# Kernel optimization log

Measured on AMD Instinct MI355X. Metric: run time of the kernel, lower is better.

The kernel has to match this reference:

```python
import jax, jax.numpy as jnp
import numpy as np

# D2Q9 lattice velocities (standard ordering: rest, axis, diagonal)
E = np.array([[0,0],[1,0],[0,1],[-1,0],[0,-1],[1,1],[-1,1],[-1,-1],[1,-1]], dtype=np.int64)

# Gram-Schmidt moment matrix, row order matches the layer's eq stack:
# [rho, jx, jy, e, eps, qx, qy, pxx, pxy]
_M_np = np.array([
    [ 1,  1,  1,  1,  1,  1,  1,  1,  1],  # rho
    [ 0,  1,  0, -1,  0,  1, -1, -1,  1],  # jx
    [ 0,  0,  1,  0, -1,  1,  1, -1, -1],  # jy
    [-4, -1, -1, -1, -1,  2,  2,  2,  2],  # e
    [ 4, -2, -2, -2, -2,  1,  1,  1,  1],  # eps
    [ 0, -2,  0,  2,  0,  1, -1, -1,  1],  # qx
    [ 0,  0, -2,  0,  2,  1,  1, -1, -1],  # qy
    [ 0,  1, -1,  1, -1,  0,  0,  0,  0],  # pxx
    [ 0,  0,  0,  0,  0,  1, -1,  1, -1],  # pxy
], dtype=np.float64)
_Minv_np = np.linalg.inv(_M_np)

TAU = 0.6
GX, GY = 0.0, -1e-4
ITERATIONS = 4
NX, NY = 1024, 1024


def _stream(f):
    # periodic streaming: shift each population along its lattice velocity
    return jnp.stack(
        [jnp.roll(f[..., i], (int(E[i, 0]), int(E[i, 1])), axis=(0, 1)) for i in range(9)],
        axis=-1,
    )


def setup_inputs() -> dict:
    key = jax.random.key(0)
    kf, kw = jax.random.split(key)
    f = jax.random.uniform(kf, (NX, NY, 9), dtype=jnp.float32)
    w = jax.random.normal(kw, (7,), dtype=jnp.float32)
    return {"f": f, "w": w}


def reference(f, w):
    M = jnp.asarray(_M_np, dtype=f.dtype)
    Minv = jnp.asarray(_Minv_np, dtype=f.dtype)
    ex = jnp.asarray(E[:, 0], dtype=f.dtype)
    ey = jnp.asarray(E[:, 1], dtype=f.dtype)
    inv_tau = jnp.asarray(1.0 / TAU, dtype=f.dtype)

    for _ in range(ITERATIONS):
        # handle_boundaries: periodic (no solid nodes) -> no-op
        f = _stream(f)
        # macroscopic fields
        rho = jnp.sum(f, axis=-1)                      # [X,Y]
        vx = jnp.einsum("xyq,q->xy", f, ex) / rho
        vy = jnp.einsum("xyq,q->xy", f, ey) / rho
        # equilibrium moments with learned coefficients (gravity forcing via tau shift)
        ux = vx + TAU * GX * rho
        uy = vy + TAU * GY * rho
        jx = rho * ux
        jy = rho * uy
        j2 = jx * jx + jy * jy
        e_m = w[0] * rho + w[1] * j2
        eps = w[2] * rho - w[3] * j2
        qx = w[4] * jx
        qy = w[4] * jy
        pxx = w[5] * (jx * jx - jy * jy)
        pxy = w[6] * jx * jy
        meq = jnp.stack([rho, jx, jy, e_m, eps, qx, qy, pxx, pxy], axis=2)
        # collision in moment space, single relaxation rate 1/tau
        m = jnp.einsum("xyq,pq->xyp", f, M)
        m = m - inv_tau * (m - meq)
        f = jnp.einsum("xyp,qp->xyq", m, Minv)
    return f
```

## Files before the change

### kernel.cpp

```cpp
#include <hip/hip_runtime.h>


#define NXD 1024
#define NYD 1024
#define NCELL (NXD * NYD)
#define ROWF (NYD * 9)

constexpr float INV_TAU = (float)(1.0 / 0.6);
constexpr float TGY     = (float)(0.6 * -1e-4);

__device__ __forceinline__ void collide1(
    float f0, float f1, float f2, float f3, float f4,
    float f5, float f6, float f7, float f8,
    float w0, float w1, float w2, float w3, float w4, float w5, float w6,
    float& o0, float& o1, float& o2, float& o3, float& o4,
    float& o5, float& o6, float& o7, float& o8)
{
    const float rho = f0 + f1 + f2 + f3 + f4 + f5 + f6 + f7 + f8;
    const float jx0 = f1 - f3 + f5 - f6 - f7 + f8;
    const float jy0 = f2 - f4 + f5 + f6 - f7 - f8;
    const float vx = jx0 / rho;
    const float vy = jy0 / rho;
    const float uy = vy + TGY * rho;
    const float jx = rho * vx;
    const float jy = rho * uy;
    const float j2 = jx * jx + jy * jy;

    const float ax = f1 + f2 + f3 + f4;
    const float dg = f5 + f6 + f7 + f8;
    const float m3 = -4.f * f0 - ax + 2.f * dg;
    const float m4 =  4.f * f0 - 2.f * ax + dg;
    const float m5 = -2.f * f1 + 2.f * f3 + f5 - f6 - f7 + f8;
    const float m6 = -2.f * f2 + 2.f * f4 + f5 + f6 - f7 - f8;
    const float m7 = f1 - f2 + f3 - f4;
    const float m8 = f5 - f6 + f7 - f8;

    const float me3 = w0 * rho + w1 * j2;
    const float me4 = w2 * rho - w3 * j2;
    const float me5 = w4 * jx;
    const float me6 = w4 * jy;
    const float me7 = w5 * (jx * jx - jy * jy);
    const float me8 = w6 * (jx * jy);

    const float mp1 = jx0 - INV_TAU * (jx0 - jx);
    const float mp2 = jy0 - INV_TAU * (jy0 - jy);
    const float mp3 = m3  - INV_TAU * (m3 - me3);
    const float mp4 = m4  - INV_TAU * (m4 - me4);
    const float mp5 = m5  - INV_TAU * (m5 - me5);
    const float mp6 = m6  - INV_TAU * (m6 - me6);
    const float mp7 = m7  - INV_TAU * (m7 - me7);
    const float mp8 = m8  - INV_TAU * (m8 - me8);

    const float s0 = rho * (1.f / 9.f);
    const float s1 = mp1 * (1.f / 6.f);
    const float s2 = mp2 * (1.f / 6.f);
    const float s3 = mp3 * (1.f / 36.f);
    const float s4 = mp4 * (1.f / 36.f);
    const float s5 = mp5 * (1.f / 12.f);
    const float s6 = mp6 * (1.f / 12.f);
    const float s7 = mp7 * 0.25f;
    const float s8 = mp8 * 0.25f;

    const float h0 = s0 - s3 - 2.f * s4;
    const float g0 = s0 + 2.f * s3 + s4;

    o0 = s0 - 4.f * s3 + 4.f * s4;
    o1 = h0 + s1 - 2.f * s5 + s7;
    o2 = h0 + s2 - 2.f * s6 - s7;
    o3 = h0 - s1 + 2.f * s5 + s7;
    o4 = h0 - s2 + 2.f * s6 - s7;
    o5 = g0 + s1 + s2 + s5 + s6 + s8;
    o6 = g0 - s1 + s2 - s5 + s6 - s8;
    o7 = g0 - s1 - s2 - s5 - s6 + s8;
    o8 = g0 + s1 - s2 + s5 - s6 - s8;
}

__device__ __forceinline__ void collide4(const float4 (&F)[9], float4 (&O)[9],
                                         const float (&w)[7]) {
    #pragma unroll
    for (int j = 0; j < 4; ++j) {
        float f[9], o[9];
        #pragma unroll
        for (int q = 0; q < 9; ++q)
            f[q] = ((const float*)&F[q])[j];
        collide1(f[0], f[1], f[2], f[3], f[4], f[5], f[6], f[7], f[8],
                 w[0], w[1], w[2], w[3], w[4], w[5], w[6],
                 o[0], o[1], o[2], o[3], o[4], o[5], o[6], o[7], o[8]);
        #pragma unroll
        for (int q = 0; q < 9; ++q)
            ((float*)&O[q])[j] = o[q];
    }
}

__device__ __forceinline__ float4 ld4s(const float* __restrict__ rowp, int yb) {
    if (yb >= 0 && yb + 3 < NYD) {
        float4 v;
        __builtin_memcpy(&v, rowp + yb, sizeof(float4));
        return v;
    }
    float4 v;
    v.x = rowp[(yb + 0) & (NYD - 1)];
    v.y = rowp[(yb + 1) & (NYD - 1)];
    v.z = rowp[(yb + 2) & (NYD - 1)];
    v.w = rowp[(yb + 3) & (NYD - 1)];
    return v;
}

__device__ __forceinline__ void pull_loads(const float* __restrict__ src,
                                           int x, int y0, float4 (&F)[9]) {
    const int xm = (x - 1) & (NXD - 1), xp = (x + 1) & (NXD - 1);
    const float* p0 = src + 0 * NCELL + x  * NYD;
    const float* p1 = src + 1 * NCELL + xm * NYD;
    const float* p2 = src + 2 * NCELL + x  * NYD;
    const float* p3 = src + 3 * NCELL + xp * NYD;
    const float* p4 = src + 4 * NCELL + x  * NYD;
    const float* p5 = src + 5 * NCELL + xm * NYD;
    const float* p6 = src + 6 * NCELL + xp * NYD;
    const float* p7 = src + 7 * NCELL + xp * NYD;
    const float* p8 = src + 8 * NCELL + xm * NYD;
    __builtin_memcpy(&F[0], p0 + y0, sizeof(float4));
    __builtin_memcpy(&F[1], p1 + y0, sizeof(float4));
    __builtin_memcpy(&F[3], p3 + y0, sizeof(float4));
    F[2] = ld4s(p2, y0 - 1);
    F[5] = ld4s(p5, y0 - 1);
    F[6] = ld4s(p6, y0 - 1);
    F[4] = ld4s(p4, y0 + 1);
    F[7] = ld4s(p7, y0 + 1);
    F[8] = ld4s(p8, y0 + 1);
}

__device__ __forceinline__ void load_w(const float* __restrict__ wp,
                                       float (&w)[7]) {
    #pragma unroll
    for (int i = 0; i < 7; ++i) w[i] = wp[i];
}

__global__ __launch_bounds__(256) void k1_sc(const float* __restrict__ src,
                                             float* __restrict__ dst,
                                             const float* __restrict__ wp) {
    __shared__ float L[3][258 * 9];
    const int b   = blockIdx.x;
    const int x   = b >> 2;
    const int y0  = (b & 3) << 8;
    const int tid = threadIdx.x;

    #pragma unroll
    for (int r = 0; r < 3; ++r) {
        const int srow = (x - 1 + r) & (NXD - 1);
        const float* rb = src + (size_t)srow * ROWF;
        const int base = y0 * 9 - 9;
        for (int p = tid; p < 258 * 9; p += 256) {
            int fr = base + p;
            if (fr < 0) fr += ROWF;
            else if (fr >= ROWF) fr -= ROWF;
            L[r][p] = rb[fr];
        }
    }
    __syncthreads();

    float w[7];
    load_w(wp, w);

    const int ly = tid;
    const int y  = y0 + ly;
    const float f0 = L[1][(ly + 1) * 9 + 0];
    const float f1 = L[0][(ly + 1) * 9 + 1];
    const float f2 = L[1][(ly + 0) * 9 + 2];
    const float f3 = L[2][(ly + 1) * 9 + 3];
    const float f4 = L[1][(ly + 2) * 9 + 4];
    const float f5 = L[0][(ly + 0) * 9 + 5];
    const float f6 = L[2][(ly + 0) * 9 + 6];
    const float f7 = L[2][(ly + 2) * 9 + 7];
    const float f8 = L[0][(ly + 2) * 9 + 8];

    float o0,o1,o2,o3,o4,o5,o6,o7,o8;
    collide1(f0,f1,f2,f3,f4,f5,f6,f7,f8,
             w[0],w[1],w[2],w[3],w[4],w[5],w[6],
             o0,o1,o2,o3,o4,o5,o6,o7,o8);

    const int c = x * NYD + y;
    dst[0 * NCELL + c] = o0;
    dst[1 * NCELL + c] = o1;
    dst[2 * NCELL + c] = o2;
    dst[3 * NCELL + c] = o3;
    dst[4 * NCELL + c] = o4;
    dst[5 * NCELL + c] = o5;
    dst[6 * NCELL + c] = o6;
    dst[7 * NCELL + c] = o7;
    dst[8 * NCELL + c] = o8;
}

__global__ __launch_bounds__(256) void k_sc(const float* __restrict__ src,
                                            float* __restrict__ dst,
                                            const float* __restrict__ wp) {
    const int x  = blockIdx.x;
    const int y0 = threadIdx.x << 2;

    float4 F[9];
    pull_loads(src, x, y0, F);

    float w[7];
    load_w(wp, w);

    float4 O[9];
    collide4(F, O, w);

    const int c = x * NYD + y0;
    #pragma unroll
    for (int q = 0; q < 9; ++q)
        *(float4*)(dst + q * NCELL + c) = O[q];
}

__global__ __launch_bounds__(256) void k_sc_aos(const float* __restrict__ src,
                                                float* __restrict__ dst,
                                                const float* __restrict__ wp) {
    __shared__ float4 T[ROWF / 4];
    const int x   = blockIdx.x;
    const int tid = threadIdx.x;
    const int y0  = tid << 2;

    float4 F[9];
    pull_loads(src, x, y0, F);

    float w[7];
    load_w(wp, w);

    float4 O[9];
    collide4(F, O, w);

    float* t = (float*)(T + tid * 9);
    #pragma unroll
    for (int j = 0; j < 4; ++j) {
        #pragma unroll
        for (int q = 0; q < 9; ++q)
            t[j * 9 + q] = ((const float*)&O[q])[j];
    }
    __syncthreads();

    float4* dv = (float4*)(dst + (size_t)x * ROWF);
    #pragma unroll
    for (int it = 0; it < 9; ++it)
        dv[tid + it * 256] = T[tid + it * 256];
}

__global__ __launch_bounds__(256) void lbm_step_aos(const float* __restrict__ src,
                                                    float* __restrict__ dst,
                                                    const float* __restrict__ wp) {
    const int cell = blockIdx.x * 256 + threadIdx.x;
    const int x = cell >> 10;
    const int y = cell & (NYD - 1);
    const int xm = (x + NXD - 1) & (NXD - 1);
    const int xp = (x + 1) & (NXD - 1);
    const int ym = (y + NYD - 1) & (NYD - 1);
    const int yp = (y + 1) & (NYD - 1);

    const float f0 = src[(x  * NYD + y ) * 9 + 0];
    const float f1 = src[(xm * NYD + y ) * 9 + 1];
    const float f2 = src[(x  * NYD + ym) * 9 + 2];
    const float f3 = src[(xp * NYD + y ) * 9 + 3];
    const float f4 = src[(x  * NYD + yp) * 9 + 4];
    const float f5 = src[(xm * NYD + ym) * 9 + 5];
    const float f6 = src[(xp * NYD + ym) * 9 + 6];
    const float f7 = src[(xp * NYD + yp) * 9 + 7];
    const float f8 = src[(xm * NYD + yp) * 9 + 8];

    float o0,o1,o2,o3,o4,o5,o6,o7,o8;
    collide1(f0,f1,f2,f3,f4,f5,f6,f7,f8,
             wp[0],wp[1],wp[2],wp[3],wp[4],wp[5],wp[6],
             o0,o1,o2,o3,o4,o5,o6,o7,o8);

    float* o = dst + (size_t)(x * NYD + y) * 9;
    o[0]=o0; o[1]=o1; o[2]=o2; o[3]=o3; o[4]=o4; o[5]=o5; o[6]=o6; o[7]=o7; o[8]=o8;
}

extern "C" void kernel_launch(void* const* d_in, const int* in_sizes, int n_in,
                              void* d_out, int out_size, void* d_ws, size_t ws_size,
                              hipStream_t stream) {
    const float* f_in = (const float*)d_in[0];
    const float* w    = (const float*)d_in[1];
    float* out = (float*)d_out;
    float* A   = (float*)d_ws;
    const size_t bufBytes = (size_t)NCELL * 9 * sizeof(float);

    if (ws_size >= 2 * bufBytes) {
        float* B = A + (size_t)NCELL * 9;
        k1_sc   <<<4096, 256, 0, stream>>>(f_in, A, w);
        k_sc    <<<1024, 256, 0, stream>>>(A, B, w);
        k_sc    <<<1024, 256, 0, stream>>>(B, A, w);
        k_sc_aos<<<1024, 256, 0, stream>>>(A, out, w);
    } else {
        float* fin_mut = (float*)d_in[0];
        lbm_step_aos<<<4096, 256, 0, stream>>>(f_in, out, w);
        lbm_step_aos<<<4096, 256, 0, stream>>>(out, fin_mut, w);
        lbm_step_aos<<<4096, 256, 0, stream>>>(fin_mut, out, w);
        lbm_step_aos<<<4096, 256, 0, stream>>>(out, fin_mut, w);
        hipMemcpyAsync(d_out, fin_mut, bufBytes, hipMemcpyDeviceToDevice, stream);
    }
}
```

Baseline: 164.0 us.

## Switch from pull-stream-collide to push collide-stream with separate transpose kernel

Replaces the pull-based stream+collide kernels with a push scheme: the first kernel only transposes AoS input to SoA while streaming, then collide-and-push kernels read aligned float4 rows and write shifted outputs, using shared memory to exchange the y-boundary lanes. Reads become fully aligned and unconditional, removing misaligned and wraparound pull loads. The cost is one extra full-grid launch (5 kernels instead of 4) with an added read/write pass, plus a block-wide barrier in every step.

```diff
diff --git a/kernel.cpp b/kernel.cpp
--- a/kernel.cpp
+++ b/kernel.cpp
@@ -12,7 +12,7 @@
 __device__ __forceinline__ void collide1(
     float f0, float f1, float f2, float f3, float f4,
     float f5, float f6, float f7, float f8,
-    float w0, float w1, float w2, float w3, float w4, float w5, float w6,
+    const float (&w)[7],
     float& o0, float& o1, float& o2, float& o3, float& o4,
     float& o5, float& o6, float& o7, float& o8)
 {
@@ -35,12 +35,12 @@
     const float m7 = f1 - f2 + f3 - f4;
     const float m8 = f5 - f6 + f7 - f8;
 
-    const float me3 = w0 * rho + w1 * j2;
-    const float me4 = w2 * rho - w3 * j2;
-    const float me5 = w4 * jx;
-    const float me6 = w4 * jy;
-    const float me7 = w5 * (jx * jx - jy * jy);
-    const float me8 = w6 * (jx * jy);
+    const float me3 = w[0] * rho + w[1] * j2;
+    const float me4 = w[2] * rho - w[3] * j2;
+    const float me5 = w[4] * jx;
+    const float me6 = w[4] * jy;
+    const float me7 = w[5] * (jx * jx - jy * jy);
+    const float me8 = w[6] * (jx * jy);
 
     const float mp1 = jx0 - INV_TAU * (jx0 - jx);
     const float mp2 = jy0 - INV_TAU * (jy0 - jy);
@@ -83,8 +83,7 @@
         #pragma unroll
         for (int q = 0; q < 9; ++q)
             f[q] = ((const float*)&F[q])[j];
-        collide1(f[0], f[1], f[2], f[3], f[4], f[5], f[6], f[7], f[8],
-                 w[0], w[1], w[2], w[3], w[4], w[5], w[6],
+        collide1(f[0], f[1], f[2], f[3], f[4], f[5], f[6], f[7], f[8], w,
                  o[0], o[1], o[2], o[3], o[4], o[5], o[6], o[7], o[8]);
         #pragma unroll
         for (int q = 0; q < 9; ++q)
@@ -92,112 +91,91 @@
     }
 }
 
-__device__ __forceinline__ float4 ld4s(const float* __restrict__ rowp, int yb) {
-    if (yb >= 0 && yb + 3 < NYD) {
-        float4 v;
-        __builtin_memcpy(&v, rowp + yb, sizeof(float4));
-        return v;
-    }
-    float4 v;
-    v.x = rowp[(yb + 0) & (NYD - 1)];
-    v.y = rowp[(yb + 1) & (NYD - 1)];
-    v.z = rowp[(yb + 2) & (NYD - 1)];
-    v.w = rowp[(yb + 3) & (NYD - 1)];
-    return v;
-}
-
-__device__ __forceinline__ void pull_loads(const float* __restrict__ src,
-                                           int x, int y0, float4 (&F)[9]) {
-    const int xm = (x - 1) & (NXD - 1), xp = (x + 1) & (NXD - 1);
-    const float* p0 = src + 0 * NCELL + x  * NYD;
-    const float* p1 = src + 1 * NCELL + xm * NYD;
-    const float* p2 = src + 2 * NCELL + x  * NYD;
-    const float* p3 = src + 3 * NCELL + xp * NYD;
-    const float* p4 = src + 4 * NCELL + x  * NYD;
-    const float* p5 = src + 5 * NCELL + xm * NYD;
-    const float* p6 = src + 6 * NCELL + xp * NYD;
-    const float* p7 = src + 7 * NCELL + xp * NYD;
-    const float* p8 = src + 8 * NCELL + xm * NYD;
-    __builtin_memcpy(&F[0], p0 + y0, sizeof(float4));
-    __builtin_memcpy(&F[1], p1 + y0, sizeof(float4));
-    __builtin_memcpy(&F[3], p3 + y0, sizeof(float4));
-    F[2] = ld4s(p2, y0 - 1);
-    F[5] = ld4s(p5, y0 - 1);
-    F[6] = ld4s(p6, y0 - 1);
-    F[4] = ld4s(p4, y0 + 1);
-    F[7] = ld4s(p7, y0 + 1);
-    F[8] = ld4s(p8, y0 + 1);
-}
-
 __device__ __forceinline__ void load_w(const float* __restrict__ wp,
                                        float (&w)[7]) {
     #pragma unroll
     for (int i = 0; i < 7; ++i) w[i] = wp[i];
 }
 
-__global__ __launch_bounds__(256) void k1_sc(const float* __restrict__ src,
-                                             float* __restrict__ dst,
-                                             const float* __restrict__ wp) {
-    __shared__ float L[3][258 * 9];
-    const int b   = blockIdx.x;
-    const int x   = b >> 2;
-    const int y0  = (b & 3) << 8;
-    const int tid = threadIdx.x;
-
-    #pragma unroll
-    for (int r = 0; r < 3; ++r) {
-        const int srow = (x - 1 + r) & (NXD - 1);
-        const float* rb = src + (size_t)srow * ROWF;
-        const int base = y0 * 9 - 9;
-        for (int p = tid; p < 258 * 9; p += 256) {
-            int fr = base + p;
-            if (fr < 0) fr += ROWF;
-            else if (fr >= ROWF) fr -= ROWF;
-            L[r][p] = rb[fr];
-        }
-    }
+__device__ __forceinline__ void push_store(float* __restrict__ dst,
+                                           const float4 (&P)[9],
+                                           float (&E)[256][7],
+                                           int x, int t) {
+    const int y0 = t << 2;
+    E[t][0] = P[2].w;  E[t][1] = P[5].w;  E[t][2] = P[6].w;
+    E[t][3] = P[4].x;  E[t][4] = P[7].x;  E[t][5] = P[8].x;
     __syncthreads();
+    const int tm = (t - 1) & 255, tp = (t + 1) & 255;
+    const float4 S2 = make_float4(E[tm][0], P[2].x, P[2].y, P[2].z);
+    const float4 S5 = make_float4(E[tm][1], P[5].x, P[5].y, P[5].z);
+    const float4 S6 = make_float4(E[tm][2], P[6].x, P[6].y, P[6].z);
+    const float4 S4 = make_float4(P[4].y, P[4].z, P[4].w, E[tp][3]);
+    const float4 S7 = make_float4(P[7].y, P[7].z, P[7].w, E[tp][4]);
+    const float4 S8 = make_float4(P[8].y, P[8].z, P[8].w, E[tp][5]);
+    const int xp = (x + 1) & (NXD - 1), xm = (x - 1) & (NXD - 1);
+    *(float4*)(dst + 0 * NCELL + x  * NYD + y0) = P[0];
+    *(float4*)(dst + 1 * NCELL + xp * NYD + y0) = P[1];
+    *(float4*)(dst + 3 * NCELL + xm * NYD + y0) = P[3];
+    *(float4*)(dst + 2 * NCELL + x  * NYD + y0) = S2;
+    *(float4*)(dst + 5 * NCELL + xp * NYD + y0) = S5;
+    *(float4*)(dst + 6 * NCELL + xm * NYD + y0) = S6;
+    *(float4*)(dst + 4 * NCELL + x  * NYD + y0) = S4;
+    *(float4*)(dst + 7 * NCELL + xm * NYD + y0) = S7;
+    *(float4*)(dst + 8 * NCELL + xp * NYD + y0) = S8;
+}
+
+__global__ __launch_bounds__(256) void k1_push(const float* __restrict__ src,
+                                               float* __restrict__ dst) {
+    __shared__ float E[256][7];
+    const int x = blockIdx.x, t = threadIdx.x;
+
+    float4 A[9];
+    const float* base = src + (size_t)x * ROWF + t * 36;
+    #pragma unroll
+    for (int q = 0; q < 9; ++q)
+        A[q] = *(const float4*)(base + 4 * q);
+
+    const float* a = (const float*)A;
+    float4 P[9];
+    #pragma unroll
+    for (int q = 0; q < 9; ++q)
+        P[q] = make_float4(a[q], a[9 + q], a[18 + q], a[27 + q]);
+
+    push_store(dst, P, E, x, t);
+}
+
+__global__ __launch_bounds__(256) void k_cs(const float* __restrict__ src,
+                                            float* __restrict__ dst,
+                                            const float* __restrict__ wp) {
+    __shared__ float E[256][7];
+    const int x = blockIdx.x, t = threadIdx.x;
+    const int y0 = t << 2;
+
+    float4 F[9];
+    #pragma unroll
+    for (int q = 0; q < 9; ++q)
+        F[q] = *(const float4*)(src + q * NCELL + x * NYD + y0);
 
     float w[7];
     load_w(wp, w);
 
-    const int ly = tid;
-    const int y  = y0 + ly;
-    const float f0 = L[1][(ly + 1) * 9 + 0];
-    const float f1 = L[0][(ly + 1) * 9 + 1];
-    const float f2 = L[1][(ly + 0) * 9 + 2];
-    const float f3 = L[2][(ly + 1) * 9 + 3];
-    const float f4 = L[1][(ly + 2) * 9 + 4];
-    const float f5 = L[0][(ly + 0) * 9 + 5];
-    const float f6 = L[2][(ly + 0) * 9 + 6];
-    const float f7 = L[2][(ly + 2) * 9 + 7];
-    const float f8 = L[0][(ly + 2) * 9 + 8];
-
-    float o0,o1,o2,o3,o4,o5,o6,o7,o8;
-    collide1(f0,f1,f2,f3,f4,f5,f6,f7,f8,
-             w[0],w[1],w[2],w[3],w[4],w[5],w[6],
-             o0,o1,o2,o3,o4,o5,o6,o7,o8);
-
-    const int c = x * NYD + y;
-    dst[0 * NCELL + c] = o0;
-    dst[1 * NCELL + c] = o1;
-    dst[2 * NCELL + c] = o2;
-    dst[3 * NCELL + c] = o3;
-    dst[4 * NCELL + c] = o4;
-    dst[5 * NCELL + c] = o5;
-    dst[6 * NCELL + c] = o6;
-    dst[7 * NCELL + c] = o7;
-    dst[8 * NCELL + c] = o8;
-}
-
-__global__ __launch_bounds__(256) void k_sc(const float* __restrict__ src,
-                                            float* __restrict__ dst,
-                                            const float* __restrict__ wp) {
-    const int x  = blockIdx.x;
-    const int y0 = threadIdx.x << 2;
+    float4 O[9];
+    collide4(F, O, w);
+
+    push_store(dst, O, E, x, t);
+}
+
+__global__ __launch_bounds__(256) void k5_aos(const float* __restrict__ src,
+                                              float* __restrict__ dst,
+                                              const float* __restrict__ wp) {
+    __shared__ float4 T[ROWF / 4];
+    const int x = blockIdx.x, t = threadIdx.x;
+    const int y0 = t << 2;
 
     float4 F[9];
-    pull_loads(src, x, y0, F);
+    #pragma unroll
+    for (int q = 0; q < 9; ++q)
+        F[q] = *(const float4*)(src + q * NCELL + x * NYD + y0);
 
     float w[7];
     load_w(wp, w);
@@ -205,42 +183,19 @@
     float4 O[9];
     collide4(F, O, w);
 
-    const int c = x * NYD + y0;
-    #pragma unroll
-    for (int q = 0; q < 9; ++q)
-        *(float4*)(dst + q * NCELL + c) = O[q];
-}
-
-__global__ __launch_bounds__(256) void k_sc_aos(const float* __restrict__ src,
-                                                float* __restrict__ dst,
-                                                const float* __restrict__ wp) {
-    __shared__ float4 T[ROWF / 4];
-    const int x   = blockIdx.x;
-    const int tid = threadIdx.x;
-    const int y0  = tid << 2;
-
-    float4 F[9];
-    pull_loads(src, x, y0, F);
-
-    float w[7];
-    load_w(wp, w);
-
-    float4 O[9];
-    collide4(F, O, w);
-
-    float* t = (float*)(T + tid * 9);
+    float* tt = (float*)(T + t * 9);
     #pragma unroll
     for (int j = 0; j < 4; ++j) {
         #pragma unroll
         for (int q = 0; q < 9; ++q)
-            t[j * 9 + q] = ((const float*)&O[q])[j];
+            tt[j * 9 + q] = ((const float*)&O[q])[j];
     }
     __syncthreads();
 
     float4* dv = (float4*)(dst + (size_t)x * ROWF);
     #pragma unroll
     for (int it = 0; it < 9; ++it)
-        dv[tid + it * 256] = T[tid + it * 256];
+        dv[t + it * 256] = T[t + it * 256];
 }
 
 __global__ __launch_bounds__(256) void lbm_step_aos(const float* __restrict__ src,
@@ -264,9 +219,10 @@
     const float f7 = src[(xp * NYD + yp) * 9 + 7];
     const float f8 = src[(xm * NYD + yp) * 9 + 8];
 
+    float w[7];
+    load_w(wp, w);
     float o0,o1,o2,o3,o4,o5,o6,o7,o8;
-    collide1(f0,f1,f2,f3,f4,f5,f6,f7,f8,
-             wp[0],wp[1],wp[2],wp[3],wp[4],wp[5],wp[6],
+    collide1(f0,f1,f2,f3,f4,f5,f6,f7,f8, w,
              o0,o1,o2,o3,o4,o5,o6,o7,o8);
 
     float* o = dst + (size_t)(x * NYD + y) * 9;
@@ -282,12 +238,15 @@
     float* A   = (float*)d_ws;
     const size_t bufBytes = (size_t)NCELL * 9 * sizeof(float);
 
+    dim3 grid(NXD), block(256);
+
     if (ws_size >= 2 * bufBytes) {
         float* B = A + (size_t)NCELL * 9;
-        k1_sc   <<<4096, 256, 0, stream>>>(f_in, A, w);
-        k_sc    <<<1024, 256, 0, stream>>>(A, B, w);
-        k_sc    <<<1024, 256, 0, stream>>>(B, A, w);
-        k_sc_aos<<<1024, 256, 0, stream>>>(A, out, w);
+        k1_push<<<grid, block, 0, stream>>>(f_in, A);
+        k_cs   <<<grid, block, 0, stream>>>(A, B, w);
+        k_cs   <<<grid, block, 0, stream>>>(B, A, w);
+        k_cs   <<<grid, block, 0, stream>>>(A, B, w);
+        k5_aos <<<grid, block, 0, stream>>>(B, out, w);
     } else {
         float* fin_mut = (float*)d_in[0];
         lbm_step_aos<<<4096, 256, 0, stream>>>(f_in, out, w);
```

Result: faster. 135.9 us (-17.2%).
